# Kernel optimization log

Measured on AMD Instinct MI355X. Metric: run time of the kernel, lower is better.

## Reference

```python
import jax, jax.numpy as jnp
import numpy as np

N, E, D, H = 8192, 8, 2048, 2048


def setup_inputs() -> dict:
    key = jax.random.key(0)
    k1, k2, k3, k4 = jax.random.split(key, 4)
    x = jax.random.normal(k1, (N, D), dtype=jnp.float32)
    indices = jax.random.randint(k2, (N, 1), 0, E)  # top_k=1 expert assignment
    W = jax.random.normal(k3, (E, D, H), dtype=jnp.float32) * 0.02
    b = jax.random.normal(k4, (E, H), dtype=jnp.float32) * 0.02
    return {"x": x, "indices": indices, "W": W, "b": b}


def reference(x, indices, W, b):
    # Each token is routed to exactly one expert (top_k=1):
    # expert_id[n] = indices[n, 0]. The torch module loops experts e=0..E-1,
    # gathers tokens with (indices == e).any(-1) (ascending order via nonzero),
    # applies expert e's Linear + ReLU, and concatenates outputs in expert order.
    expert_id = indices[:, 0]                              # [N]
    # Dense dispatch: compute every expert's linear on every token, then pick
    # each token's own expert row (jit-friendly; no data-dependent shapes).
    y_all = jnp.einsum('nd,edh->neh', x, W) + b[None, :, :]  # [N, E, H]
    y = jnp.take_along_axis(y_all, expert_id[:, None, None], axis=1)[:, 1 - 1, :]  # [N, H]
    y = jax.nn.relu(y)
    # Concat in expert order == stable sort of tokens by expert id
    # (nonzero returns ascending indices, so within-expert order is preserved).
    order = jnp.argsort(expert_id)  # stable by default
    return y[order]
```

## Files before the change

### kernel.cpp

```cpp
#include <hip/hip_runtime.h>

#define N_TOK 8192
#define N_EXP 8
#define DIM   2048
#define HID   2048

typedef __attribute__((ext_vector_type(8))) short short8;
typedef __attribute__((ext_vector_type(4))) float f32x4;
typedef __attribute__((ext_vector_type(4))) unsigned short ushort4v;

__device__ inline unsigned short f2bf(float f) {
  unsigned int u = __builtin_bit_cast(unsigned int, f);
  unsigned int r = u + 0x7FFFu + ((u >> 16) & 1u);
  return (unsigned short)(r >> 16);
}

__global__ __launch_bounds__(256) void sort_experts(const int* __restrict__ idx,
                                                    int* __restrict__ perm,
                                                    int* __restrict__ offs) {
  __shared__ int cnt[256][8];
  __shared__ int base[8];
  const int t = threadIdx.x;
  int local[8] = {0,0,0,0,0,0,0,0};
  const int r0 = t * 32;
  for (int i = 0; i < 32; ++i) {
    int e = idx[r0 + i] & 7;
    ++local[e];
  }
#pragma unroll
  for (int e = 0; e < 8; ++e) cnt[t][e] = local[e];
  __syncthreads();
  if (t < 8) {
    int s = 0;
    for (int i = 0; i < 256; ++i) { int v = cnt[i][t]; cnt[i][t] = s; s += v; }
    base[t] = s;
  }
  __syncthreads();
  if (t == 0) {
    int s = 0;
    for (int e = 0; e < 8; ++e) { int v = base[e]; offs[e] = s; base[e] = s; s += v; }
    offs[8] = s;
  }
  __syncthreads();
  int pos[8];
#pragma unroll
  for (int e = 0; e < 8; ++e) pos[e] = base[e] + cnt[t][e];
  for (int i = 0; i < 32; ++i) {
    int r = r0 + i;
    int e = idx[r] & 7;
    perm[pos[e]++] = r;
  }
}

__global__ __launch_bounds__(256) void gather_convert_x(const float* __restrict__ x,
                                                        const int* __restrict__ perm,
                                                        unsigned short* __restrict__ xs) {
  int gid = blockIdx.x * 256 + threadIdx.x;
  int p = gid >> 8;
  int c = gid & 255;
  int src = perm[p];
  const float* sp = x + (size_t)src * DIM + c * 8;
  float4 a = *(const float4*)sp;
  float4 b = *(const float4*)(sp + 4);
  short8 o;
  o[0] = (short)f2bf(a.x); o[1] = (short)f2bf(a.y);
  o[2] = (short)f2bf(a.z); o[3] = (short)f2bf(a.w);
  o[4] = (short)f2bf(b.x); o[5] = (short)f2bf(b.y);
  o[6] = (short)f2bf(b.z); o[7] = (short)f2bf(b.w);
  *(short8*)(xs + (size_t)p * DIM + c * 8) = o;
}

__global__ __launch_bounds__(256) void transpose_convert_w(const float* __restrict__ W,
                                                           unsigned short* __restrict__ Wt) {
  __shared__ unsigned short tile[64][68];
  const int e = blockIdx.z;
  const int d0 = blockIdx.y * 64;
  const int h0 = blockIdx.x * 64;
  const int t = threadIdx.x;
  const int cr = t & 15;
  const int rr = t >> 4;
  const float* Wp = W + ((size_t)e * DIM + d0) * HID + h0;
#pragma unroll
  for (int i = 0; i < 4; ++i) {
    int d = rr + i * 16;
    float4 v = *(const float4*)(Wp + (size_t)d * HID + cr * 4);
    ushort4v o;
    o[0] = f2bf(v.x); o[1] = f2bf(v.y); o[2] = f2bf(v.z); o[3] = f2bf(v.w);
    *(ushort4v*)&tile[d][cr * 4] = o;
  }
  __syncthreads();
  unsigned short* op = Wt + ((size_t)e * HID + h0) * DIM + d0;
#pragma unroll
  for (int i = 0; i < 4; ++i) {
    int h = rr + i * 16;
    ushort4v o;
    o[0] = tile[cr * 4 + 0][h];
    o[1] = tile[cr * 4 + 1][h];
    o[2] = tile[cr * 4 + 2][h];
    o[3] = tile[cr * 4 + 3][h];
    *(ushort4v*)(op + (size_t)h * DIM + cr * 4) = o;
  }
}

#define BM 128
#define BN 128
#define BK 32

__global__ __launch_bounds__(256) void grouped_gemm(const unsigned short* __restrict__ xs,
                                                    const unsigned short* __restrict__ Wt,
                                                    const float* __restrict__ bias,
                                                    const int* __restrict__ offs,
                                                    float* __restrict__ out) {
  const int e   = blockIdx.z;
  const int off = offs[e];
  const int cnt = offs[e + 1] - off;
  const int mt  = blockIdx.y;
  if (mt * BM >= cnt) return;
  const int n0 = blockIdx.x * BN;

  __shared__ __align__(16) unsigned short As[BM * BK];
  __shared__ __align__(16) unsigned short Bs[BN * BK];

  const int t    = threadIdx.x;
  const int wid  = t >> 6;
  const int lane = t & 63;
  const int wr   = wid >> 1, wc = wid & 1;
  const int l15  = lane & 15;
  const int l4   = lane >> 4;

  f32x4 acc[4][4] = {};

  size_t srcA[2], srcB[2];
  const size_t WtE = (size_t)e * DIM * HID;
#pragma unroll
  for (int c = 0; c < 2; ++c) {
    int lin = c * 256 + t;
    int r = lin >> 2, kq = lin & 3;
    int p = off + mt * BM + r;
    if (p > N_TOK - 1) p = N_TOK - 1;
    srcA[c] = (size_t)p * DIM + kq * 8;
    srcB[c] = WtE + (size_t)(n0 + r) * DIM + kq * 8;
  }

  for (int k0 = 0; k0 < DIM; k0 += BK) {
#pragma unroll
    for (int c = 0; c < 2; ++c) {
      __builtin_amdgcn_global_load_lds(
          (const __attribute__((address_space(1))) void*)(xs + srcA[c] + k0),
          (__attribute__((address_space(3))) void*)(As + c * 2048 + t * 8), 16, 0, 0);
      __builtin_amdgcn_global_load_lds(
          (const __attribute__((address_space(1))) void*)(Wt + srcB[c] + k0),
          (__attribute__((address_space(3))) void*)(Bs + c * 2048 + t * 8), 16, 0, 0);
    }
    __syncthreads();

    short8 af[4], bf[4];
#pragma unroll
    for (int m = 0; m < 4; ++m) {
      int row = wr * 64 + m * 16 + l15;
      af[m] = *(const short8*)(As + row * BK + l4 * 8);
    }
#pragma unroll
    for (int n = 0; n < 4; ++n) {
      int row = wc * 64 + n * 16 + l15;
      bf[n] = *(const short8*)(Bs + row * BK + l4 * 8);
    }
#pragma unroll
    for (int m = 0; m < 4; ++m)
#pragma unroll
      for (int n = 0; n < 4; ++n)
        acc[m][n] = __builtin_amdgcn_mfma_f32_16x16x32_bf16(af[m], bf[n], acc[m][n], 0, 0, 0);
    __syncthreads();
  }

#pragma unroll
  for (int n = 0; n < 4; ++n) {
    int col = n0 + wc * 64 + n * 16 + l15;
    float bv = bias[e * HID + col];
#pragma unroll
    for (int m = 0; m < 4; ++m) {
#pragma unroll
      for (int q = 0; q < 4; ++q) {
        int rl = wr * 64 + m * 16 + l4 * 4 + q;
        if (mt * BM + rl < cnt) {
          float v = acc[m][n][q] + bv;
          out[(size_t)(off + mt * BM + rl) * HID + col] = v > 0.f ? v : 0.f;
        }
      }
    }
  }
}

extern "C" void kernel_launch(void* const* d_in, const int* in_sizes, int n_in,
                              void* d_out, int out_size, void* d_ws, size_t ws_size,
                              hipStream_t stream) {
  const float* x   = (const float*)d_in[0];
  const int*   idx = (const int*)d_in[1];
  const float* W   = (const float*)d_in[2];
  const float* b   = (const float*)d_in[3];
  float* out = (float*)d_out;

  char* ws = (char*)d_ws;
  unsigned short* xs = (unsigned short*)ws;
  unsigned short* Wt = (unsigned short*)(ws + (size_t)N_TOK * DIM * 2);
  int* perm = (int*)(ws + (size_t)N_TOK * DIM * 2 + (size_t)N_EXP * DIM * HID * 2);
  int* offs = perm + N_TOK;

  sort_experts<<<1, 256, 0, stream>>>(idx, perm, offs);
  gather_convert_x<<<N_TOK * (DIM / 8) / 256, 256, 0, stream>>>(x, perm, xs);
  transpose_convert_w<<<dim3(HID / 64, DIM / 64, N_EXP), 256, 0, stream>>>(W, Wt);
  grouped_gemm<<<dim3(HID / BN, N_TOK / BM, N_EXP), 256, 0, stream>>>(xs, Wt, b, offs, out);
}
```

Measured before the change: 188.6 us.

## Enlarge GEMM tiles to 256x256 with 4-stage LDS pipeline and swizzle

Rewrites the grouped GEMM main loop. Tiles grow to 256x256 with 512 threads (8 waves, each computing a 128x64 sub-tile), and a 4-deep ring of LDS buffers is filled by direct global-to-LDS loads issued three K-steps ahead, with explicit vmcnt waits and s_setprio around the MFMA bursts. LDS addresses are XOR-swizzled to avoid bank conflicts. The aim is to hide load latency and raise arithmetic intensity per loaded byte. In exchange the kernel uses more registers and a large LDS footprint. The bigger M tiles also waste more work on partially filled per-expert tiles and give fewer blocks in the grid.

Measured after the change: 207.5 us. +10.0%, slower.

```diff
diff --git a/kernel.cpp b/kernel.cpp
--- a/kernel.cpp
+++ b/kernel.cpp
@@ -102,15 +102,17 @@
   }
 }
 
-#define BM 128
-#define BN 128
+#define BM 256
+#define BN 256
 #define BK 32
-
-__global__ __launch_bounds__(256) void grouped_gemm(const unsigned short* __restrict__ xs,
-                                                    const unsigned short* __restrict__ Wt,
-                                                    const float* __restrict__ bias,
-                                                    const int* __restrict__ offs,
-                                                    float* __restrict__ out) {
+#define NTILE (DIM / BK)
+
+__global__ __launch_bounds__(512, 2) void grouped_gemm(
+    const unsigned short* __restrict__ xs,
+    const unsigned short* __restrict__ Wt,
+    const float* __restrict__ bias,
+    const int* __restrict__ offs,
+    float* __restrict__ out) {
   const int e   = blockIdx.z;
   const int off = offs[e];
   const int cnt = offs[e + 1] - off;
@@ -118,59 +120,151 @@
   if (mt * BM >= cnt) return;
   const int n0 = blockIdx.x * BN;
 
-  __shared__ __align__(16) unsigned short As[BM * BK];
-  __shared__ __align__(16) unsigned short Bs[BN * BK];
+  __shared__ __align__(16) unsigned short sm[4 * 2 * 8192];
 
   const int t    = threadIdx.x;
+  const int lane = t & 63;
   const int wid  = t >> 6;
-  const int lane = t & 63;
-  const int wr   = wid >> 1, wc = wid & 1;
+  const int wr   = wid >> 2;
+  const int wc   = wid & 3;
   const int l15  = lane & 15;
   const int l4   = lane >> 4;
 
-  f32x4 acc[4][4] = {};
-
-  size_t srcA[2], srcB[2];
+  int aOff0, aOff1, aOff2, aOff3, aOff4, aOff5, aOff6, aOff7;
+  int bOff0, bOff1, bOff2, bOff3;
+  {
+    int ao[8], bo[4];
+#pragma unroll
+    for (int m = 0; m < 8; ++m) {
+      int row = wr * 128 + m * 16 + l15;
+      int o = row * 64 + l4 * 16;
+      o ^= ((o >> 7) & 3) << 4;
+      ao[m] = o >> 1;
+    }
+#pragma unroll
+    for (int n = 0; n < 4; ++n) {
+      int col = wc * 64 + n * 16 + l15;
+      int o = col * 64 + l4 * 16;
+      o ^= ((o >> 7) & 3) << 4;
+      bo[n] = o >> 1;
+    }
+    aOff0=ao[0]; aOff1=ao[1]; aOff2=ao[2]; aOff3=ao[3];
+    aOff4=ao[4]; aOff5=ao[5]; aOff6=ao[6]; aOff7=ao[7];
+    bOff0=bo[0]; bOff1=bo[1]; bOff2=bo[2]; bOff3=bo[3];
+  }
+
   const size_t WtE = (size_t)e * DIM * HID;
-#pragma unroll
-  for (int c = 0; c < 2; ++c) {
-    int lin = c * 256 + t;
-    int r = lin >> 2, kq = lin & 3;
-    int p = off + mt * BM + r;
-    if (p > N_TOK - 1) p = N_TOK - 1;
-    srcA[c] = (size_t)p * DIM + kq * 8;
-    srcB[c] = WtE + (size_t)(n0 + r) * DIM + kq * 8;
-  }
-
-  for (int k0 = 0; k0 < DIM; k0 += BK) {
+  const int aBase = off + mt * BM;
+  size_t sA0, sA1, sB0, sB1;
+  int ldsOff0, ldsOff1;
+  {
+    size_t sa[2], sb[2]; int lo[2];
 #pragma unroll
     for (int c = 0; c < 2; ++c) {
-      __builtin_amdgcn_global_load_lds(
-          (const __attribute__((address_space(1))) void*)(xs + srcA[c] + k0),
-          (__attribute__((address_space(3))) void*)(As + c * 2048 + t * 8), 16, 0, 0);
-      __builtin_amdgcn_global_load_lds(
-          (const __attribute__((address_space(1))) void*)(Wt + srcB[c] + k0),
-          (__attribute__((address_space(3))) void*)(Bs + c * 2048 + t * 8), 16, 0, 0);
+      int o  = (c * 512 + t) * 16;
+      int so = o ^ (((o >> 7) & 3) << 4);
+      int row = so >> 6;
+      int kb  = (so & 63) >> 1;
+      int p = aBase + row; if (p > N_TOK - 1) p = N_TOK - 1;
+      sa[c] = (size_t)p * DIM + kb;
+      sb[c] = WtE + (size_t)(n0 + row) * DIM + kb;
+      lo[c] = (c * 512 + t) * 8;
     }
-    __syncthreads();
-
-    short8 af[4], bf[4];
-#pragma unroll
-    for (int m = 0; m < 4; ++m) {
-      int row = wr * 64 + m * 16 + l15;
-      af[m] = *(const short8*)(As + row * BK + l4 * 8);
-    }
-#pragma unroll
-    for (int n = 0; n < 4; ++n) {
-      int row = wc * 64 + n * 16 + l15;
-      bf[n] = *(const short8*)(Bs + row * BK + l4 * 8);
-    }
-#pragma unroll
-    for (int m = 0; m < 4; ++m)
-#pragma unroll
-      for (int n = 0; n < 4; ++n)
-        acc[m][n] = __builtin_amdgcn_mfma_f32_16x16x32_bf16(af[m], bf[n], acc[m][n], 0, 0, 0);
-    __syncthreads();
+    sA0 = sa[0]; sA1 = sa[1]; sB0 = sb[0]; sB1 = sb[1];
+    ldsOff0 = lo[0]; ldsOff1 = lo[1];
+  }
+
+  auto stageA = [&](int T_) {
+    int bsl = (T_ & 3) * 2;
+    int kofs = T_ * BK;
+    __builtin_amdgcn_global_load_lds(
+        (const __attribute__((address_space(1))) void*)(xs + sA0 + kofs),
+        (__attribute__((address_space(3))) void*)(sm + bsl * 8192 + ldsOff0), 16, 0, 0);
+    __builtin_amdgcn_global_load_lds(
+        (const __attribute__((address_space(1))) void*)(xs + sA1 + kofs),
+        (__attribute__((address_space(3))) void*)(sm + bsl * 8192 + ldsOff1), 16, 0, 0);
+  };
+  auto stageB = [&](int T_) {
+    int bsl = (T_ & 3) * 2 + 1;
+    int kofs = T_ * BK;
+    __builtin_amdgcn_global_load_lds(
+        (const __attribute__((address_space(1))) void*)(Wt + sB0 + kofs),
+        (__attribute__((address_space(3))) void*)(sm + bsl * 8192 + ldsOff0), 16, 0, 0);
+    __builtin_amdgcn_global_load_lds(
+        (const __attribute__((address_space(1))) void*)(Wt + sB1 + kofs),
+        (__attribute__((address_space(3))) void*)(sm + bsl * 8192 + ldsOff1), 16, 0, 0);
+  };
+
+  f32x4 acc[8][4] = {};
+
+  stageA(0); stageB(0); stageA(1); stageB(1); stageA(2); stageB(2);
+  asm volatile("s_waitcnt vmcnt(8)" ::: "memory");
+  __builtin_amdgcn_s_barrier();
+
+  short8 b0, b1, b2, b3;
+  for (int T = 0; T < NTILE; ++T) {
+    const unsigned short* LA = sm + (T & 3) * 16384;
+    const unsigned short* LB = LA + 8192;
+    short8 a0, a1, a2, a3;
+
+    a0 = *(const short8*)(LA + aOff0);
+    a1 = *(const short8*)(LA + aOff1);
+    a2 = *(const short8*)(LA + aOff2);
+    a3 = *(const short8*)(LA + aOff3);
+    b0 = *(const short8*)(LB + bOff0);
+    b1 = *(const short8*)(LB + bOff1);
+    b2 = *(const short8*)(LB + bOff2);
+    b3 = *(const short8*)(LB + bOff3);
+    if (T < NTILE - 3) stageA(T + 3);
+    __builtin_amdgcn_s_barrier();
+    __builtin_amdgcn_s_setprio(1);
+    acc[0][0] = __builtin_amdgcn_mfma_f32_16x16x32_bf16(a0, b0, acc[0][0], 0, 0, 0);
+    acc[0][1] = __builtin_amdgcn_mfma_f32_16x16x32_bf16(a0, b1, acc[0][1], 0, 0, 0);
+    acc[0][2] = __builtin_amdgcn_mfma_f32_16x16x32_bf16(a0, b2, acc[0][2], 0, 0, 0);
+    acc[0][3] = __builtin_amdgcn_mfma_f32_16x16x32_bf16(a0, b3, acc[0][3], 0, 0, 0);
+    acc[1][0] = __builtin_amdgcn_mfma_f32_16x16x32_bf16(a1, b0, acc[1][0], 0, 0, 0);
+    acc[1][1] = __builtin_amdgcn_mfma_f32_16x16x32_bf16(a1, b1, acc[1][1], 0, 0, 0);
+    acc[1][2] = __builtin_amdgcn_mfma_f32_16x16x32_bf16(a1, b2, acc[1][2], 0, 0, 0);
+    acc[1][3] = __builtin_amdgcn_mfma_f32_16x16x32_bf16(a1, b3, acc[1][3], 0, 0, 0);
+    acc[2][0] = __builtin_amdgcn_mfma_f32_16x16x32_bf16(a2, b0, acc[2][0], 0, 0, 0);
+    acc[2][1] = __builtin_amdgcn_mfma_f32_16x16x32_bf16(a2, b1, acc[2][1], 0, 0, 0);
+    acc[2][2] = __builtin_amdgcn_mfma_f32_16x16x32_bf16(a2, b2, acc[2][2], 0, 0, 0);
+    acc[2][3] = __builtin_amdgcn_mfma_f32_16x16x32_bf16(a2, b3, acc[2][3], 0, 0, 0);
+    acc[3][0] = __builtin_amdgcn_mfma_f32_16x16x32_bf16(a3, b0, acc[3][0], 0, 0, 0);
+    acc[3][1] = __builtin_amdgcn_mfma_f32_16x16x32_bf16(a3, b1, acc[3][1], 0, 0, 0);
+    acc[3][2] = __builtin_amdgcn_mfma_f32_16x16x32_bf16(a3, b2, acc[3][2], 0, 0, 0);
+    acc[3][3] = __builtin_amdgcn_mfma_f32_16x16x32_bf16(a3, b3, acc[3][3], 0, 0, 0);
+    __builtin_amdgcn_s_setprio(0);
+    __builtin_amdgcn_s_barrier();
+
+    a0 = *(const short8*)(LA + aOff4);
+    a1 = *(const short8*)(LA + aOff5);
+    a2 = *(const short8*)(LA + aOff6);
+    a3 = *(const short8*)(LA + aOff7);
+    if (T < NTILE - 3) stageB(T + 3);
+    __builtin_amdgcn_s_barrier();
+    __builtin_amdgcn_s_setprio(1);
+    acc[4][0] = __builtin_amdgcn_mfma_f32_16x16x32_bf16(a0, b0, acc[4][0], 0, 0, 0);
+    acc[4][1] = __builtin_amdgcn_mfma_f32_16x16x32_bf16(a0, b1, acc[4][1], 0, 0, 0);
+    acc[4][2] = __builtin_amdgcn_mfma_f32_16x16x32_bf16(a0, b2, acc[4][2], 0, 0, 0);
+    acc[4][3] = __builtin_amdgcn_mfma_f32_16x16x32_bf16(a0, b3, acc[4][3], 0, 0, 0);
+    acc[5][0] = __builtin_amdgcn_mfma_f32_16x16x32_bf16(a1, b0, acc[5][0], 0, 0, 0);
+    acc[5][1] = __builtin_amdgcn_mfma_f32_16x16x32_bf16(a1, b1, acc[5][1], 0, 0, 0);
+    acc[5][2] = __builtin_amdgcn_mfma_f32_16x16x32_bf16(a1, b2, acc[5][2], 0, 0, 0);
+    acc[5][3] = __builtin_amdgcn_mfma_f32_16x16x32_bf16(a1, b3, acc[5][3], 0, 0, 0);
+    acc[6][0] = __builtin_amdgcn_mfma_f32_16x16x32_bf16(a2, b0, acc[6][0], 0, 0, 0);
+    acc[6][1] = __builtin_amdgcn_mfma_f32_16x16x32_bf16(a2, b1, acc[6][1], 0, 0, 0);
+    acc[6][2] = __builtin_amdgcn_mfma_f32_16x16x32_bf16(a2, b2, acc[6][2], 0, 0, 0);
+    acc[6][3] = __builtin_amdgcn_mfma_f32_16x16x32_bf16(a2, b3, acc[6][3], 0, 0, 0);
+    acc[7][0] = __builtin_amdgcn_mfma_f32_16x16x32_bf16(a3, b0, acc[7][0], 0, 0, 0);
+    acc[7][1] = __builtin_amdgcn_mfma_f32_16x16x32_bf16(a3, b1, acc[7][1], 0, 0, 0);
+    acc[7][2] = __builtin_amdgcn_mfma_f32_16x16x32_bf16(a3, b2, acc[7][2], 0, 0, 0);
+    acc[7][3] = __builtin_amdgcn_mfma_f32_16x16x32_bf16(a3, b3, acc[7][3], 0, 0, 0);
+    __builtin_amdgcn_s_setprio(0);
+    if (T < NTILE - 3)       { asm volatile("s_waitcnt vmcnt(8)" ::: "memory"); }
+    else if (T == NTILE - 3) { asm volatile("s_waitcnt vmcnt(4)" ::: "memory"); }
+    else if (T == NTILE - 2) { asm volatile("s_waitcnt vmcnt(0)" ::: "memory"); }
+    __builtin_amdgcn_s_barrier();
   }
 
 #pragma unroll
@@ -178,13 +272,13 @@
     int col = n0 + wc * 64 + n * 16 + l15;
     float bv = bias[e * HID + col];
 #pragma unroll
-    for (int m = 0; m < 4; ++m) {
+    for (int m = 0; m < 8; ++m) {
 #pragma unroll
       for (int q = 0; q < 4; ++q) {
-        int rl = wr * 64 + m * 16 + l4 * 4 + q;
-        if (mt * BM + rl < cnt) {
+        int r = wr * 128 + m * 16 + l4 * 4 + q;
+        if (mt * BM + r < cnt) {
           float v = acc[m][n][q] + bv;
-          out[(size_t)(off + mt * BM + rl) * HID + col] = v > 0.f ? v : 0.f;
+          out[(size_t)(off + mt * BM + r) * HID + col] = v > 0.f ? v : 0.f;
         }
       }
     }
@@ -209,5 +303,5 @@
   sort_experts<<<1, 256, 0, stream>>>(idx, perm, offs);
   gather_convert_x<<<N_TOK * (DIM / 8) / 256, 256, 0, stream>>>(x, perm, xs);
   transpose_convert_w<<<dim3(HID / 64, DIM / 64, N_EXP), 256, 0, stream>>>(W, Wt);
-  grouped_gemm<<<dim3(HID / BN, N_TOK / BM, N_EXP), 256, 0, stream>>>(xs, Wt, b, offs, out);
-}
+  grouped_gemm<<<dim3(HID / BN, N_TOK / BM, N_EXP), 512, 0, stream>>>(xs, Wt, b, offs, out);
+}
```

## Rewrite grouped GEMM as 256x256 tile, double-buffered, swizzled LDS pipeline

Applied to the files above, without the earlier changes.

Replaces the 128x128x32 single-buffered grouped GEMM with a 512-thread, 256x256 output tile kernel whose 64-wide K chunks are double-buffered in LDS. Global-to-LDS loads are interleaved with MFMA phases using explicit barriers, vmcnt waits and setprio. An XOR swizzle on LDS columns is meant to avoid bank conflicts. This targets the exposed load latency and the low operand reuse of the old kernel. The cost is 128KB of LDS per block, a large register accumulator, and more wasted work on partial expert tiles because the M tile is bigger.

Measured after the change: 195.8 us. +3.9%, slower.

```diff
diff --git a/kernel.cpp b/kernel.cpp
--- a/kernel.cpp
+++ b/kernel.cpp
@@ -102,75 +102,162 @@
   }
 }
 
-#define BM 128
-#define BN 128
-#define BK 32
-
-__global__ __launch_bounds__(256) void grouped_gemm(const unsigned short* __restrict__ xs,
-                                                    const unsigned short* __restrict__ Wt,
-                                                    const float* __restrict__ bias,
-                                                    const int* __restrict__ offs,
-                                                    float* __restrict__ out) {
+#define NK    32
+#define NITER 16
+
+#define MM(D,A,B) D = __builtin_amdgcn_mfma_f32_16x16x32_bf16(A, B, D, 0, 0, 0)
+#define GLD(SRC, DST) __builtin_amdgcn_global_load_lds( \
+    (const __attribute__((address_space(1))) void*)(SRC), \
+    (__attribute__((address_space(3))) void*)(DST), 16, 0, 0)
+#define BAR() __builtin_amdgcn_s_barrier()
+#define PRIO(x) __builtin_amdgcn_s_setprio(x)
+
+#define ST_A(SLOT,Q,KOFS) do { \
+    GLD(xs + paw0##Q + (KOFS), sm + (SLOT)*32768 + (Q)*4096 + 0*8192 + dA); \
+    GLD(xs + paw1##Q + (KOFS), sm + (SLOT)*32768 + (Q)*4096 + 1*8192 + dA); } while(0)
+#define ST_B(SLOT,HH,KOFS) do { \
+    GLD(Wt + pbw0##HH + (KOFS), sm + (SLOT)*32768 + 16384 + (HH)*8192 + 0*4096 + dA); \
+    GLD(Wt + pbw1##HH + (KOFS), sm + (SLOT)*32768 + 16384 + (HH)*8192 + 1*4096 + dA); } while(0)
+
+#define READ_A(LS, MH, CB) \
+    fa0 = *(const short8*)((LS) + arow + ((MH)*4+0)*1024 + (CB)); \
+    fa1 = *(const short8*)((LS) + arow + ((MH)*4+1)*1024 + (CB)); \
+    fa2 = *(const short8*)((LS) + arow + ((MH)*4+2)*1024 + (CB)); \
+    fa3 = *(const short8*)((LS) + arow + ((MH)*4+3)*1024 + (CB));
+
+#define READ_B(LS, CB, B0,B1,B2,B3) \
+    B0 = *(const short8*)((LS) + brow + 0*1024 + (CB)); \
+    B1 = *(const short8*)((LS) + brow + 1*1024 + (CB)); \
+    B2 = *(const short8*)((LS) + brow + 2*1024 + (CB)); \
+    B3 = *(const short8*)((LS) + brow + 3*1024 + (CB));
+
+#define QUAD(MB, B0,B1,B2,B3) \
+    MM(acc[MB+0][0],fa0,B0); MM(acc[MB+0][1],fa0,B1); MM(acc[MB+0][2],fa0,B2); MM(acc[MB+0][3],fa0,B3); \
+    MM(acc[MB+1][0],fa1,B0); MM(acc[MB+1][1],fa1,B1); MM(acc[MB+1][2],fa1,B2); MM(acc[MB+1][3],fa1,B3); \
+    MM(acc[MB+2][0],fa2,B0); MM(acc[MB+2][1],fa2,B1); MM(acc[MB+2][2],fa2,B2); MM(acc[MB+2][3],fa2,B3); \
+    MM(acc[MB+3][0],fa3,B0); MM(acc[MB+3][1],fa3,B1); MM(acc[MB+3][2],fa3,B2); MM(acc[MB+3][3],fa3,B3);
+
+__global__ __launch_bounds__(512, 2) void grouped_gemm(
+    const unsigned short* __restrict__ xs,
+    const unsigned short* __restrict__ Wt,
+    const float* __restrict__ bias,
+    const int* __restrict__ offs,
+    float* __restrict__ out) {
   const int e   = blockIdx.z;
   const int off = offs[e];
   const int cnt = offs[e + 1] - off;
   const int mt  = blockIdx.y;
-  if (mt * BM >= cnt) return;
-  const int n0 = blockIdx.x * BN;
-
-  __shared__ __align__(16) unsigned short As[BM * BK];
-  __shared__ __align__(16) unsigned short Bs[BN * BK];
+  if (mt * 256 >= cnt) return;
+  const int n0 = blockIdx.x * 256;
+
+  __shared__ __align__(16) unsigned short sm[65536];
 
   const int t    = threadIdx.x;
+  const int lane = t & 63;
   const int wid  = t >> 6;
-  const int lane = t & 63;
-  const int wr   = wid >> 1, wc = wid & 1;
+  const int wr   = wid >> 2;
+  const int wc   = wid & 3;
   const int l15  = lane & 15;
   const int l4   = lane >> 4;
 
-  f32x4 acc[4][4] = {};
-
-  size_t srcA[2], srcB[2];
-  const size_t WtE = (size_t)e * DIM * HID;
-#pragma unroll
-  for (int c = 0; c < 2; ++c) {
-    int lin = c * 256 + t;
-    int r = lin >> 2, kq = lin & 3;
-    int p = off + mt * BM + r;
-    if (p > N_TOK - 1) p = N_TOK - 1;
-    srcA[c] = (size_t)p * DIM + kq * 8;
-    srcB[c] = WtE + (size_t)(n0 + r) * DIM + kq * 8;
-  }
-
-  for (int k0 = 0; k0 < DIM; k0 += BK) {
-#pragma unroll
-    for (int c = 0; c < 2; ++c) {
-      __builtin_amdgcn_global_load_lds(
-          (const __attribute__((address_space(1))) void*)(xs + srcA[c] + k0),
-          (__attribute__((address_space(3))) void*)(As + c * 2048 + t * 8), 16, 0, 0);
-      __builtin_amdgcn_global_load_lds(
-          (const __attribute__((address_space(1))) void*)(Wt + srcB[c] + k0),
-          (__attribute__((address_space(3))) void*)(Bs + c * 2048 + t * 8), 16, 0, 0);
-    }
-    __syncthreads();
-
-    short8 af[4], bf[4];
-#pragma unroll
-    for (int m = 0; m < 4; ++m) {
-      int row = wr * 64 + m * 16 + l15;
-      af[m] = *(const short8*)(As + row * BK + l4 * 8);
-    }
-#pragma unroll
-    for (int n = 0; n < 4; ++n) {
-      int row = wc * 64 + n * 16 + l15;
-      bf[n] = *(const short8*)(Bs + row * BK + l4 * 8);
-    }
-#pragma unroll
-    for (int m = 0; m < 4; ++m)
-#pragma unroll
-      for (int n = 0; n < 4; ++n)
-        acc[m][n] = __builtin_amdgcn_mfma_f32_16x16x32_bf16(af[m], bf[n], acc[m][n], 0, 0, 0);
-    __syncthreads();
+  const int cb0  = (l4 * 8) ^ ((l15 & 7) << 3);
+  const int cb1  = cb0 ^ 32;
+  const int arow = (wr * 128 + l15) * 64;
+  const int brow = 16384 + (wc * 64 + l15) * 64;
+
+  const int r0  = t >> 3;
+  const int keu = ((t & 7) * 8) ^ ((r0 & 7) << 3);
+  const int aBase = off + mt * 256;
+  const int dA = t * 8;
+
+  unsigned int paw00, paw10, paw01, paw11, pbw00, pbw10, pbw01, pbw11;
+  {
+    int p;
+    p = aBase + 0*128 + 0*64 + r0; if (p > N_TOK-1) p = N_TOK-1; paw00 = (unsigned)p*2048 + keu;
+    p = aBase + 1*128 + 0*64 + r0; if (p > N_TOK-1) p = N_TOK-1; paw10 = (unsigned)p*2048 + keu;
+    p = aBase + 0*128 + 1*64 + r0; if (p > N_TOK-1) p = N_TOK-1; paw01 = (unsigned)p*2048 + keu;
+    p = aBase + 1*128 + 1*64 + r0; if (p > N_TOK-1) p = N_TOK-1; paw11 = (unsigned)p*2048 + keu;
+    unsigned int eW = (unsigned)e * (DIM * HID);
+    pbw00 = eW + (unsigned)(n0 + 0*128 + 0*64 + r0) * 2048 + keu;
+    pbw10 = eW + (unsigned)(n0 + 0*128 + 1*64 + r0) * 2048 + keu;
+    pbw01 = eW + (unsigned)(n0 + 1*128 + 0*64 + r0) * 2048 + keu;
+    pbw11 = eW + (unsigned)(n0 + 1*128 + 1*64 + r0) * 2048 + keu;
+  }
+
+  f32x4 acc[8][4] = {};
+  const unsigned short* S0 = sm;
+  const unsigned short* S1 = sm + 32768;
+
+  ST_A(0,0,0); ST_B(0,0,0); ST_B(0,1,0); ST_A(0,1,0);
+  ST_A(1,0,64); ST_B(1,0,64);
+  asm volatile("s_waitcnt vmcnt(4)" ::: "memory");
+  BAR();
+
+  short8 fa0, fa1, fa2, fa3;
+  short8 bk00, bk01, bk02, bk03;
+  short8 bk10, bk11, bk12, bk13;
+
+#pragma unroll 1
+  for (int i = 0; i < NITER; ++i) {
+    const int kc = i * 128;
+    const bool nl = (i < NITER - 1);
+
+    READ_A(S0, 0, cb0);
+    READ_B(S0, cb0, bk00, bk01, bk02, bk03);
+    ST_B(1,1,kc+64);
+    BAR(); PRIO(1);
+    QUAD(0, bk00, bk01, bk02, bk03);
+    PRIO(0); BAR();
+
+    READ_A(S0, 0, cb1);
+    READ_B(S0, cb1, bk10, bk11, bk12, bk13);
+    ST_A(1,1,kc+64);
+    BAR(); PRIO(1);
+    QUAD(0, bk10, bk11, bk12, bk13);
+    PRIO(0); BAR();
+
+    READ_A(S0, 1, cb0);
+    if (nl) ST_A(0,0,kc+128);
+    BAR(); PRIO(1);
+    QUAD(4, bk00, bk01, bk02, bk03);
+    PRIO(0); BAR();
+
+    READ_A(S0, 1, cb1);
+    if (nl) ST_B(0,0,kc+128);
+    BAR(); PRIO(1);
+    QUAD(4, bk10, bk11, bk12, bk13);
+    PRIO(0);
+    if (nl) { asm volatile("s_waitcnt vmcnt(4)" ::: "memory"); }
+    else    { asm volatile("s_waitcnt vmcnt(0)" ::: "memory"); }
+    BAR();
+
+    READ_A(S1, 0, cb0);
+    READ_B(S1, cb0, bk00, bk01, bk02, bk03);
+    if (nl) ST_B(0,1,kc+128);
+    BAR(); PRIO(1);
+    QUAD(0, bk00, bk01, bk02, bk03);
+    PRIO(0); BAR();
+
+    READ_A(S1, 0, cb1);
+    READ_B(S1, cb1, bk10, bk11, bk12, bk13);
+    if (nl) ST_A(0,1,kc+128);
+    BAR(); PRIO(1);
+    QUAD(0, bk10, bk11, bk12, bk13);
+    PRIO(0); BAR();
+
+    READ_A(S1, 1, cb0);
+    if (nl) ST_A(1,0,kc+192);
+    BAR(); PRIO(1);
+    QUAD(4, bk00, bk01, bk02, bk03);
+    PRIO(0); BAR();
+
+    READ_A(S1, 1, cb1);
+    if (nl) ST_B(1,0,kc+192);
+    BAR(); PRIO(1);
+    QUAD(4, bk10, bk11, bk12, bk13);
+    PRIO(0);
+    if (nl) { asm volatile("s_waitcnt vmcnt(4)" ::: "memory"); }
+    BAR();
   }
 
 #pragma unroll
@@ -178,13 +265,13 @@
     int col = n0 + wc * 64 + n * 16 + l15;
     float bv = bias[e * HID + col];
 #pragma unroll
-    for (int m = 0; m < 4; ++m) {
+    for (int m = 0; m < 8; ++m) {
 #pragma unroll
       for (int q = 0; q < 4; ++q) {
-        int rl = wr * 64 + m * 16 + l4 * 4 + q;
-        if (mt * BM + rl < cnt) {
+        int r = wr * 128 + m * 16 + l4 * 4 + q;
+        if (mt * 256 + r < cnt) {
           float v = acc[m][n][q] + bv;
-          out[(size_t)(off + mt * BM + rl) * HID + col] = v > 0.f ? v : 0.f;
+          out[(size_t)(off + mt * 256 + r) * HID + col] = v > 0.f ? v : 0.f;
         }
       }
     }
@@ -209,5 +296,5 @@
   sort_experts<<<1, 256, 0, stream>>>(idx, perm, offs);
   gather_convert_x<<<N_TOK * (DIM / 8) / 256, 256, 0, stream>>>(x, perm, xs);
   transpose_convert_w<<<dim3(HID / 64, DIM / 64, N_EXP), 256, 0, stream>>>(W, Wt);
-  grouped_gemm<<<dim3(HID / BN, N_TOK / BM, N_EXP), 256, 0, stream>>>(xs, Wt, b, offs, out);
-}
+  grouped_gemm<<<dim3(HID / 256, N_TOK / 256, N_EXP), 512, 0, stream>>>(xs, Wt, b, offs, out);
+}
```

## Rewrite grouped GEMM with triple-buffered LDS pipeline, swizzle, 128x256 tiles

Applied to the files above, without the earlier changes.

Restructures the grouped GEMM into 512-thread blocks computing 128x256 tiles with BK=64, triple-buffered LDS slots filled by async global-to-LDS loads issued two k-steps ahead. LDS columns are XOR-swizzled to avoid bank conflicts, and each k-step is split into two half-steps that interleave loads with MFMA bursts under raised wave priority. The aim is to hide global memory latency and cut barrier stalls, in exchange for far more LDS per block (144KB) and more complex waitcnt bookkeeping.

After: 182.6 us. -3.1%, faster.

```diff
diff --git a/kernel.cpp b/kernel.cpp
--- a/kernel.cpp
+++ b/kernel.cpp
@@ -102,75 +102,121 @@
   }
 }
 
-#define BM 128
-#define BN 128
-#define BK 32
-
-__global__ __launch_bounds__(256) void grouped_gemm(const unsigned short* __restrict__ xs,
-                                                    const unsigned short* __restrict__ Wt,
-                                                    const float* __restrict__ bias,
-                                                    const int* __restrict__ offs,
-                                                    float* __restrict__ out) {
+#define NKT 32
+#define SLOT_USH 24576
+
+#define MM(D,A,B) D = __builtin_amdgcn_mfma_f32_16x16x32_bf16(A, B, D, 0, 0, 0)
+#define GLD(SRC, DST) __builtin_amdgcn_global_load_lds( \
+    (const __attribute__((address_space(1))) void*)(SRC), \
+    (__attribute__((address_space(3))) void*)(DST), 16, 0, 0)
+#define BAR() __builtin_amdgcn_s_barrier()
+#define PRIO(x) __builtin_amdgcn_s_setprio(x)
+
+__global__ __launch_bounds__(512, 2) void grouped_gemm(
+    const unsigned short* __restrict__ xs,
+    const unsigned short* __restrict__ Wt,
+    const float* __restrict__ bias,
+    const int* __restrict__ offs,
+    float* __restrict__ out) {
   const int e   = blockIdx.z;
   const int off = offs[e];
   const int cnt = offs[e + 1] - off;
   const int mt  = blockIdx.y;
-  if (mt * BM >= cnt) return;
-  const int n0 = blockIdx.x * BN;
-
-  __shared__ __align__(16) unsigned short As[BM * BK];
-  __shared__ __align__(16) unsigned short Bs[BN * BK];
+  if (mt * 128 >= cnt) return;
+  const int n0 = blockIdx.x * 256;
+
+  __shared__ __align__(16) unsigned short sm[3 * SLOT_USH];
 
   const int t    = threadIdx.x;
+  const int lane = t & 63;
   const int wid  = t >> 6;
-  const int lane = t & 63;
-  const int wr   = wid >> 1, wc = wid & 1;
+  const int wr   = wid >> 2;
+  const int wc   = wid & 3;
   const int l15  = lane & 15;
   const int l4   = lane >> 4;
 
+  const int cb0  = (l4 * 8) ^ ((l15 & 7) << 3);
+  const int cb1  = cb0 ^ 32;
+  const int arow = (wr * 64 + l15) * 64;
+  const int brow = 8192 + (wc * 64 + l15) * 64;
+
+  const int r0  = t >> 3;
+  const int keu = ((t & 7) * 8) ^ ((r0 & 7) << 3);
+  const int aBase = off + mt * 128;
+  const int dA = t * 8;
+
+  unsigned int pa0, pa1, pb0, pb1, pb2, pb3;
+  {
+    int p;
+    p = aBase + 0 * 64 + r0; if (p > N_TOK - 1) p = N_TOK - 1; pa0 = (unsigned)p * 2048 + keu;
+    p = aBase + 1 * 64 + r0; if (p > N_TOK - 1) p = N_TOK - 1; pa1 = (unsigned)p * 2048 + keu;
+    unsigned int eW = (unsigned)e * (DIM * HID);
+    pb0 = eW + (unsigned)(n0 + 0 * 64 + r0) * 2048 + keu;
+    pb1 = eW + (unsigned)(n0 + 1 * 64 + r0) * 2048 + keu;
+    pb2 = eW + (unsigned)(n0 + 2 * 64 + r0) * 2048 + keu;
+    pb3 = eW + (unsigned)(n0 + 3 * 64 + r0) * 2048 + keu;
+  }
+
+#define ST_A(SBASE, KOFS) do { \
+    GLD(xs + pa0 + (KOFS), sm + (SBASE) + 0 * 4096 + dA); \
+    GLD(xs + pa1 + (KOFS), sm + (SBASE) + 1 * 4096 + dA); } while (0)
+#define ST_B0(SBASE, KOFS) GLD(Wt + pb0 + (KOFS), sm + (SBASE) + 8192 + 0 * 4096 + dA)
+#define ST_B123(SBASE, KOFS) do { \
+    GLD(Wt + pb1 + (KOFS), sm + (SBASE) + 8192 + 1 * 4096 + dA); \
+    GLD(Wt + pb2 + (KOFS), sm + (SBASE) + 8192 + 2 * 4096 + dA); \
+    GLD(Wt + pb3 + (KOFS), sm + (SBASE) + 8192 + 3 * 4096 + dA); } while (0)
+
+#define READ_FRAGS(SP, CB) \
+    fa0 = *(const short8*)((SP) + arow + 0 * 1024 + (CB)); \
+    fa1 = *(const short8*)((SP) + arow + 1 * 1024 + (CB)); \
+    fa2 = *(const short8*)((SP) + arow + 2 * 1024 + (CB)); \
+    fa3 = *(const short8*)((SP) + arow + 3 * 1024 + (CB)); \
+    fb0 = *(const short8*)((SP) + brow + 0 * 1024 + (CB)); \
+    fb1 = *(const short8*)((SP) + brow + 1 * 1024 + (CB)); \
+    fb2 = *(const short8*)((SP) + brow + 2 * 1024 + (CB)); \
+    fb3 = *(const short8*)((SP) + brow + 3 * 1024 + (CB));
+
+#define MFMA16() \
+    MM(acc[0][0],fa0,fb0); MM(acc[0][1],fa0,fb1); MM(acc[0][2],fa0,fb2); MM(acc[0][3],fa0,fb3); \
+    MM(acc[1][0],fa1,fb0); MM(acc[1][1],fa1,fb1); MM(acc[1][2],fa1,fb2); MM(acc[1][3],fa1,fb3); \
+    MM(acc[2][0],fa2,fb0); MM(acc[2][1],fa2,fb1); MM(acc[2][2],fa2,fb2); MM(acc[2][3],fa2,fb3); \
+    MM(acc[3][0],fa3,fb0); MM(acc[3][1],fa3,fb1); MM(acc[3][2],fa3,fb2); MM(acc[3][3],fa3,fb3);
+
   f32x4 acc[4][4] = {};
 
-  size_t srcA[2], srcB[2];
-  const size_t WtE = (size_t)e * DIM * HID;
-#pragma unroll
-  for (int c = 0; c < 2; ++c) {
-    int lin = c * 256 + t;
-    int r = lin >> 2, kq = lin & 3;
-    int p = off + mt * BM + r;
-    if (p > N_TOK - 1) p = N_TOK - 1;
-    srcA[c] = (size_t)p * DIM + kq * 8;
-    srcB[c] = WtE + (size_t)(n0 + r) * DIM + kq * 8;
-  }
-
-  for (int k0 = 0; k0 < DIM; k0 += BK) {
-#pragma unroll
-    for (int c = 0; c < 2; ++c) {
-      __builtin_amdgcn_global_load_lds(
-          (const __attribute__((address_space(1))) void*)(xs + srcA[c] + k0),
-          (__attribute__((address_space(3))) void*)(As + c * 2048 + t * 8), 16, 0, 0);
-      __builtin_amdgcn_global_load_lds(
-          (const __attribute__((address_space(1))) void*)(Wt + srcB[c] + k0),
-          (__attribute__((address_space(3))) void*)(Bs + c * 2048 + t * 8), 16, 0, 0);
-    }
-    __syncthreads();
-
-    short8 af[4], bf[4];
-#pragma unroll
-    for (int m = 0; m < 4; ++m) {
-      int row = wr * 64 + m * 16 + l15;
-      af[m] = *(const short8*)(As + row * BK + l4 * 8);
-    }
-#pragma unroll
-    for (int n = 0; n < 4; ++n) {
-      int row = wc * 64 + n * 16 + l15;
-      bf[n] = *(const short8*)(Bs + row * BK + l4 * 8);
-    }
-#pragma unroll
-    for (int m = 0; m < 4; ++m)
-#pragma unroll
-      for (int n = 0; n < 4; ++n)
-        acc[m][n] = __builtin_amdgcn_mfma_f32_16x16x32_bf16(af[m], bf[n], acc[m][n], 0, 0, 0);
-    __syncthreads();
+  ST_A(0, 0); ST_B0(0, 0); ST_B123(0, 0);
+  ST_A(SLOT_USH, 64); ST_B0(SLOT_USH, 64); ST_B123(SLOT_USH, 64);
+  asm volatile("s_waitcnt vmcnt(6)" ::: "memory");
+  BAR();
+
+  short8 fa0, fa1, fa2, fa3, fb0, fb1, fb2, fb3;
+  int sl = 0;
+  int s2 = 2;
+
+#pragma unroll 1
+  for (int T = 0; T < NKT; ++T) {
+    const unsigned short* SP = sm + sl * SLOT_USH;
+    const int sb = s2 * SLOT_USH;
+    const int kofs = (T + 2) * 64;
+    const bool st = (T < NKT - 2);
+
+    READ_FRAGS(SP, cb0);
+    if (st) { ST_A(sb, kofs); ST_B0(sb, kofs); }
+    BAR(); PRIO(1);
+    MFMA16();
+    PRIO(0); BAR();
+
+    READ_FRAGS(SP, cb1);
+    if (st) { ST_B123(sb, kofs); }
+    BAR(); PRIO(1);
+    MFMA16();
+    PRIO(0);
+    if (T < NKT - 2)       { asm volatile("s_waitcnt vmcnt(6)" ::: "memory"); }
+    else if (T == NKT - 2) { asm volatile("s_waitcnt vmcnt(0)" ::: "memory"); }
+    BAR();
+
+    sl = (sl == 2) ? 0 : sl + 1;
+    s2 = (s2 == 2) ? 0 : s2 + 1;
   }
 
 #pragma unroll
@@ -181,10 +227,10 @@
     for (int m = 0; m < 4; ++m) {
 #pragma unroll
       for (int q = 0; q < 4; ++q) {
-        int rl = wr * 64 + m * 16 + l4 * 4 + q;
-        if (mt * BM + rl < cnt) {
+        int r = wr * 64 + m * 16 + l4 * 4 + q;
+        if (mt * 128 + r < cnt) {
           float v = acc[m][n][q] + bv;
-          out[(size_t)(off + mt * BM + rl) * HID + col] = v > 0.f ? v : 0.f;
+          out[(size_t)(off + mt * 128 + r) * HID + col] = v > 0.f ? v : 0.f;
         }
       }
     }
@@ -209,5 +255,5 @@
   sort_experts<<<1, 256, 0, stream>>>(idx, perm, offs);
   gather_convert_x<<<N_TOK * (DIM / 8) / 256, 256, 0, stream>>>(x, perm, xs);
   transpose_convert_w<<<dim3(HID / 64, DIM / 64, N_EXP), 256, 0, stream>>>(W, Wt);
-  grouped_gemm<<<dim3(HID / BN, N_TOK / BM, N_EXP), 256, 0, stream>>>(xs, Wt, b, offs, out);
-}
+  grouped_gemm<<<dim3(HID / 256, N_TOK / 128, N_EXP), 512, 0, stream>>>(xs, Wt, b, offs, out);
+}
```
